# Optimization experiments

Measured on AMD Instinct MI355X. Metric: run time of the kernel, lower is better.

## Reference

```python
import jax, jax.numpy as jnp
import numpy as np
import math

D = 256; NH = 8; NG = 64; META = 6

def _linear(x, w, b):
    return x @ w.T + b

def setup_inputs():
    key = jax.random.key(0)
    ks = jax.random.split(key, 12)
    B, T, TG = 32, 4096, 1024
    def rn(k, shape, s=0.02):
        return jax.random.normal(k, shape, dtype=jnp.float32) * s
    q = jax.random.normal(ks[0], (1, NG, D), dtype=jnp.float32)
    q = q / jnp.clip(jnp.linalg.norm(q, axis=-1, keepdims=True), 1e-6)
    # fibonacci unit sphere anchor, scaled by 0.4
    idx = jnp.arange(NG, dtype=jnp.float32)
    golden = (1.0 + math.sqrt(5.0)) / 2.0
    theta = 2.0 * math.pi * idx / golden
    z = jnp.clip(1.0 - (2.0 * idx + 1.0) / NG, -1.0 + 1e-6, 1.0 - 1e-6)
    r = jnp.sqrt(jnp.clip(1.0 - z * z, 0.0))
    pts = jnp.stack([r * jnp.cos(theta), r * jnp.sin(theta), z], axis=-1)
    pts = pts / jnp.clip(jnp.linalg.norm(pts, axis=-1, keepdims=True), 1e-6)
    p0 = (pts * 0.4)[None]
    ph_b2 = jnp.array([0.0] * 6 + [-2.0] * 4, dtype=jnp.float32)
    return dict(
        local_feat=jax.random.normal(ks[1], (B, D, T), dtype=jnp.float32),
        global_feat=jax.random.normal(ks[2], (B, D, TG), dtype=jnp.float32),
        meta=jax.random.uniform(ks[3], (B, META), dtype=jnp.float32),
        queries=q, p0_anchor=p0,
        in_proj_w=rn(ks[4], (3 * D, D)), in_proj_b=jnp.zeros((3 * D,), jnp.float32),
        out_proj_w=rn(ks[5], (D, D)), out_proj_b=jnp.zeros((D,), jnp.float32),
        ln_g=jnp.ones((D,), jnp.float32), ln_b=jnp.zeros((D,), jnp.float32),
        meta_w=rn(ks[6], (D, META)), meta_b=jnp.zeros((D,), jnp.float32),
        temporal_w=rn(ks[7], (D, D)), temporal_b=jnp.zeros((D,), jnp.float32),
        shift_w=rn(ks[8], (3, D)), shift_b=jnp.zeros((3,), jnp.float32),
        ph_w1=rn(ks[9], (D // 2, D)), ph_b1=jnp.zeros((D // 2,), jnp.float32),
        ph_w2=rn(ks[10], (10, D // 2)), ph_b2=ph_b2,
        wave_delay_scale=jnp.float32(0.1),
        envelope_bias=jnp.float32(0.5),
    )

def reference(local_feat, global_feat, meta, queries, p0_anchor, in_proj_w, in_proj_b,
              out_proj_w, out_proj_b, ln_g, ln_b, meta_w, meta_b, temporal_w, temporal_b,
              shift_w, shift_b, ph_w1, ph_b1, ph_w2, ph_b2, wave_delay_scale, envelope_bias):
    B, _, T = local_feat.shape
    DH = D // NH
    kv = jnp.transpose(global_feat, (0, 2, 1))                        # [B,TG,D]
    q = jnp.broadcast_to(queries, (B, NG, D))
    wq, wk, wv = in_proj_w[:D], in_proj_w[D:2 * D], in_proj_w[2 * D:]
    bq, bk, bv = in_proj_b[:D], in_proj_b[D:2 * D], in_proj_b[2 * D:]
    qh = _linear(q, wq, bq).reshape(B, NG, NH, DH)
    kh = _linear(kv, wk, bk).reshape(B, -1, NH, DH)
    vh = _linear(kv, wv, bv).reshape(B, -1, NH, DH)
    attn = jax.nn.softmax(jnp.einsum('bqhd,bkhd->bhqk', qh, kh) / math.sqrt(DH), axis=-1)
    ctx = jnp.einsum('bhqk,bkhd->bqhd', attn, vh).reshape(B, NG, D)
    x = q + _linear(ctx, out_proj_w, out_proj_b)
    mu = x.mean(-1, keepdims=True)
    var = ((x - mu) ** 2).mean(-1, keepdims=True)
    q_static = (x - mu) / jnp.sqrt(var + 1e-5) * ln_g + ln_b
    q_static = q_static + jax.nn.gelu(_linear(meta, meta_w, meta_b), approximate=False)[:, None, :]
    params = _linear(jax.nn.gelu(_linear(q_static, ph_w1, ph_b1), approximate=False), ph_w2, ph_b2)
    p0_delta = jnp.tanh(params[..., 0:3]) * 0.2
    heart_shift = jnp.tanh(_linear(global_feat.mean(-1), shift_w, shift_b)) * 0.3
    p_pos = p0_anchor + p0_delta + heart_shift[:, None, :]            # [B,NG,3]
    dnorm = jnp.clip(jnp.linalg.norm(params[..., 3:6], axis=-1, keepdims=True), 1e-6)
    dipole_dir = params[..., 3:6] / dnorm
    volume_xyz = jax.nn.sigmoid(params[..., 6:9]) * 0.5 + 0.001
    amplitude = jax.nn.sigmoid(params[..., 9]) + 1e-4                 # [B,NG]
    tw = _linear(q_static, temporal_w, temporal_b)                    # [B,NG,D]
    temporal_logits = jnp.einsum('bnc,bct->bnt', tw, local_feat) / math.sqrt(D)
    idx_sa = jnp.argmax(amplitude, axis=1)                            # [B]
    p_sa = jnp.take_along_axis(p_pos, idx_sa[:, None, None], axis=1)  # [B,1,3]
    dist = jnp.linalg.norm(p_pos - p_sa, axis=-1)                     # [B,NG]
    delay = jnp.clip(jax.nn.softplus(wave_delay_scale) * dist, 0.0, 0.1)
    base_x = jnp.linspace(-1.0, 1.0, T)
    grid_x = base_x[None, None, :] - delay[..., None]                 # [B,NG,T]
    # grid_sample(bilinear, zeros, align_corners=True): grid_y hits rows exactly,
    # so it reduces to 1D linear interp along time with zero padding.
    x_pix = (grid_x + 1.0) * 0.5 * (T - 1)
    x0 = jnp.floor(x_pix).astype(jnp.int32)
    x1 = x0 + 1
    w1 = x_pix - x0.astype(x_pix.dtype)
    w0 = 1.0 - w1
    def samp(xi):
        g = jnp.take_along_axis(temporal_logits, jnp.clip(xi, 0, T - 1), axis=-1)
        return g * ((xi >= 0) & (xi <= T - 1)).astype(g.dtype)
    shifted = w0 * samp(x0) + w1 * samp(x1)
    envelope_t = jax.nn.sigmoid(shifted + envelope_bias)              # [B,NG,T]
    return amplitude, p_pos, dipole_dir, volume_xyz, envelope_t
```

## Files before the change

### kernel.cpp

```cpp
#include <hip/hip_runtime.h>
#include <hip/hip_bf16.h>
#include <math.h>

typedef __hip_bfloat16 bf16;
typedef short s16x8 __attribute__((ext_vector_type(8)));
typedef float f32x4 __attribute__((ext_vector_type(4)));

#define NDIM 256
#define NTG 1024
#define NT 4096

__device__ __forceinline__ float gelu_exact(float x) {
    return 0.5f * x * (1.0f + erff(x * 0.70710678118654752440f));
}
__device__ __forceinline__ float sigmoidf_(float x) {
    return 1.0f / (1.0f + __expf(-x));
}
__device__ __forceinline__ short f2bf_s(float x) {
    union { bf16 h; short s; } cv;
    cv.h = __float2bfloat16(x);
    return cv.s;
}
__device__ __forceinline__ float bf2f(short s) {
    union { bf16 h; short s; } cv;
    cv.s = s;
    return __bfloat162float(cv.h);
}

__global__ __launch_bounds__(256) void k_prep(
        const float* __restrict__ gf, const float* __restrict__ ipw,
        const float* __restrict__ opw, const float* __restrict__ twm,
        const float* __restrict__ pw1, const float* __restrict__ queries,
        const float* __restrict__ ipb,
        bf16* __restrict__ gfT, float* __restrict__ partial,
        float* __restrict__ opwT, float* __restrict__ twT, float* __restrict__ pw1T,
        bf16* __restrict__ wkvK, bf16* __restrict__ wkvV,
        float* __restrict__ qh) {
    __shared__ float smem[64 * 65 + 256];
    int blk = blockIdx.x, tid = threadIdx.x;
    if (blk < 2048) {
        float (*tile)[65] = (float(*)[65])smem;
        float* psum = smem + 64 * 65;
        int t0 = (blk & 15) * 64, c0 = ((blk >> 4) & 3) * 64, b = blk >> 6;
        int tt = tid & 63, ci = tid >> 6;
        #pragma unroll
        for (int r = 0; r < 16; ++r) {
            int cl = ci * 16 + r;
            tile[cl][tt] = gf[((size_t)(b * 256 + c0 + cl)) * NTG + t0 + tt];
        }
        __syncthreads();
        int cc = tid & 63, ti = tid >> 6;
        #pragma unroll
        for (int r = 0; r < 16; ++r) {
            int tl = ti * 16 + r;
            gfT[((size_t)(b * 1024 + t0 + tl)) * 256 + c0 + cc] =
                __float2bfloat16(tile[cc][tl]);
        }
        float ps = 0.f;
        #pragma unroll
        for (int r = 0; r < 16; ++r) ps += tile[cc][ti * 16 + r];
        psum[tid] = ps;
        __syncthreads();
        if (tid < 64) {
            float s = psum[tid] + psum[tid + 64] + psum[tid + 128] + psum[tid + 192];
            partial[(b * 256 + c0 + tid) * 16 + (blk & 15)] = s;
        }
    } else {
        int pblk = blk - 2048;
        if (pblk < 384) {
            int id = pblk * 256 + tid;
            if (id < 65536) {
                int k = id >> 8, c = id & 255;
                opwT[id] = opw[c * 256 + k];
                twT[id]  = twm[c * 256 + k];
            } else {
                int id2 = id - 65536;
                int k = id2 >> 7, m = id2 & 127;
                pw1T[id2] = pw1[m * 256 + k];
            }
        } else if (pblk < 640) {
            int id = (pblk - 384) * 256 + tid;
            wkvK[id] = __float2bfloat16(ipw[65536 + id]);
            wkvV[id] = __float2bfloat16(ipw[131072 + id]);
        } else {
            float* qrow = smem;
            int n = pblk - 640, c = tid;
            qrow[c] = queries[n * 256 + c];
            __syncthreads();
            float s = ipb[c];
            const float* wr = ipw + c * 256;
            for (int k = 0; k < 256; ++k) s += qrow[k] * wr[k];
            qh[n * 256 + c] = s;
        }
    }
}

__global__ __launch_bounds__(256) void k_kv(
        const short* __restrict__ gfT, const short* __restrict__ wkvK,
        const short* __restrict__ wkvV, const float* __restrict__ ipb,
        const float* __restrict__ meta, const float* __restrict__ mw,
        const float* __restrict__ mb, const float* __restrict__ partial,
        const float* __restrict__ sw, const float* __restrict__ sb,
        short* __restrict__ kvh, short* __restrict__ vTg,
        float* __restrict__ metag, float* __restrict__ hshift) {
    int blk = blockIdx.x;
    int tid = threadIdx.x;
    if (blk >= 512) {
        __shared__ float gm[256];
        int b = blk - 512, c = tid;
        float m = 0.f;
        const float* pp = partial + (b * 256 + c) * 16;
        #pragma unroll
        for (int tt = 0; tt < 16; ++tt) m += pp[tt];
        gm[c] = m * (1.0f / 1024.0f);
        float s = mb[c];
        #pragma unroll
        for (int j = 0; j < 6; ++j) s += meta[b * 6 + j] * mw[c * 6 + j];
        metag[b * 256 + c] = gelu_exact(s);
        __syncthreads();
        if (c < 3) {
            float t = sb[c];
            for (int k = 0; k < 256; ++k) t += gm[k] * sw[c * 256 + k];
            hshift[b * 4 + c] = tanhf(t) * 0.3f;
        }
        return;
    }
    int w = tid >> 6, lane = tid & 63, lm = lane & 15, quad = lane >> 4;
    int bx = blk & 7, sel = (blk >> 3) & 1, b = blk >> 4;
    int t0 = bx * 128 + w * 32;
    s16x8 g[8][2];
    #pragma unroll
    for (int ks = 0; ks < 8; ++ks) {
        int c = ks * 32 + quad * 8;
        #pragma unroll
        for (int mt = 0; mt < 2; ++mt)
            g[ks][mt] = *(const s16x8*)&gfT[((size_t)(b * 1024 + t0 + mt * 16 + lm)) * 256 + c];
    }
    if (sel == 0) {
        for (int n0i = 0; n0i < 4; ++n0i) {
            int n0 = n0i * 64;
            f32x4 acc[4][2];
            #pragma unroll
            for (int ni = 0; ni < 4; ++ni)
                #pragma unroll
                for (int mt = 0; mt < 2; ++mt) acc[ni][mt] = (f32x4)(0.0f);
            #pragma unroll
            for (int ks = 0; ks < 8; ++ks) {
                int c = ks * 32 + quad * 8;
                #pragma unroll
                for (int ni = 0; ni < 4; ++ni) {
                    s16x8 aw = *(const s16x8*)&wkvK[(n0 + ni * 16 + lm) * 256 + c];
                    #pragma unroll
                    for (int mt = 0; mt < 2; ++mt)
                        acc[ni][mt] = __builtin_amdgcn_mfma_f32_16x16x32_bf16(aw, g[ks][mt], acc[ni][mt], 0, 0, 0);
                }
            }
            #pragma unroll
            for (int ni = 0; ni < 4; ++ni) {
                int nb4 = n0 + ni * 16 + quad * 4;
                float4 bias = *(const float4*)&ipb[256 + nb4];
                #pragma unroll
                for (int mt = 0; mt < 2; ++mt) {
                    int t = t0 + mt * 16 + lm;
                    ushort4 o;
                    o.x = (unsigned short)f2bf_s(acc[ni][mt][0] + bias.x);
                    o.y = (unsigned short)f2bf_s(acc[ni][mt][1] + bias.y);
                    o.z = (unsigned short)f2bf_s(acc[ni][mt][2] + bias.z);
                    o.w = (unsigned short)f2bf_s(acc[ni][mt][3] + bias.w);
                    *(ushort4*)&kvh[((size_t)(b * 1024 + t)) * 256 + nb4] = o;
                }
            }
        }
    } else {
        for (int n0i = 0; n0i < 4; ++n0i) {
            int n0 = n0i * 64;
            f32x4 acc[2][4];
            #pragma unroll
            for (int mt = 0; mt < 2; ++mt)
                #pragma unroll
                for (int ni = 0; ni < 4; ++ni) acc[mt][ni] = (f32x4)(0.0f);
            #pragma unroll
            for (int ks = 0; ks < 8; ++ks) {
                int c = ks * 32 + quad * 8;
                #pragma unroll
                for (int ni = 0; ni < 4; ++ni) {
                    s16x8 bw = *(const s16x8*)&wkvV[(n0 + ni * 16 + lm) * 256 + c];
                    #pragma unroll
                    for (int mt = 0; mt < 2; ++mt)
                        acc[mt][ni] = __builtin_amdgcn_mfma_f32_16x16x32_bf16(g[ks][mt], bw, acc[mt][ni], 0, 0, 0);
                }
            }
            #pragma unroll
            for (int ni = 0; ni < 4; ++ni) {
                int nv = n0 + ni * 16 + lm;
                float bias = ipb[512 + nv];
                #pragma unroll
                for (int mt = 0; mt < 2; ++mt) {
                    int t4 = t0 + mt * 16 + quad * 4;
                    ushort4 o;
                    o.x = (unsigned short)f2bf_s(acc[mt][ni][0] + bias);
                    o.y = (unsigned short)f2bf_s(acc[mt][ni][1] + bias);
                    o.z = (unsigned short)f2bf_s(acc[mt][ni][2] + bias);
                    o.w = (unsigned short)f2bf_s(acc[mt][ni][3] + bias);
                    *(ushort4*)&vTg[((size_t)(b * 256 + nv)) * 1024 + t4] = o;
                }
            }
        }
    }
}

__global__ __launch_bounds__(256) void k_attn(
        const short* __restrict__ kvh, const short* __restrict__ vTg,
        const float* __restrict__ qh,
        float* __restrict__ o_half, float* __restrict__ l_half) {
    __shared__ short pT[4][64 * 40];
    __shared__ float obuf[4][64 * 36];
    __shared__ float lbuf[4 * 64];
    int tid = threadIdx.x;
    int w = tid >> 6, lane = tid & 63, lm = lane & 15, quad = lane >> 4;
    int half = blockIdx.x, h = blockIdx.y, b = blockIdx.z;
    s16x8 aq[4];
    #pragma unroll
    for (int mt = 0; mt < 4; ++mt) {
        const float4* qp = (const float4*)(qh + (mt * 16 + lm) * 256 + h * 32 + quad * 8);
        float4 qa = qp[0], qb = qp[1];
        aq[mt][0] = f2bf_s(qa.x); aq[mt][1] = f2bf_s(qa.y);
        aq[mt][2] = f2bf_s(qa.z); aq[mt][3] = f2bf_s(qa.w);
        aq[mt][4] = f2bf_s(qb.x); aq[mt][5] = f2bf_s(qb.y);
        aq[mt][6] = f2bf_s(qb.z); aq[mt][7] = f2bf_s(qb.w);
    }
    f32x4 acco[2][4];
    #pragma unroll
    for (int dt = 0; dt < 2; ++dt)
        #pragma unroll
        for (int qt = 0; qt < 4; ++qt) acco[dt][qt] = (f32x4)(0.0f);
    float lp[4][4];
    #pragma unroll
    for (int mt = 0; mt < 4; ++mt)
        #pragma unroll
        for (int r = 0; r < 4; ++r) lp[mt][r] = 0.f;
    const float scale = 0.17677669529663687f;
    int kb = half * 512 + w * 128;
    for (int ch = 0; ch < 4; ++ch) {
        int n0 = kb + ch * 32;
        #pragma unroll
        for (int nt = 0; nt < 2; ++nt) {
            int key = n0 + nt * 16 + lm;
            s16x8 bk = *(const s16x8*)&kvh[((size_t)(b * 1024 + key)) * 256 + h * 32 + quad * 8];
            f32x4 zero = {0.f, 0.f, 0.f, 0.f};
            #pragma unroll
            for (int mt = 0; mt < 4; ++mt) {
                f32x4 S = __builtin_amdgcn_mfma_f32_16x16x32_bf16(aq[mt], bk, zero, 0, 0, 0);
                #pragma unroll
                for (int r = 0; r < 4; ++r) {
                    float e = __expf(S[r] * scale);
                    lp[mt][r] += e;
                    pT[w][(mt * 16 + quad * 4 + r) * 40 + nt * 16 + lm] = f2bf_s(e);
                }
            }
        }
        s16x8 av[2], bp[4];
        #pragma unroll
        for (int dt = 0; dt < 2; ++dt)
            av[dt] = *(const s16x8*)&vTg[((size_t)(b * 256 + h * 32 + dt * 16 + lm)) * 1024 + n0 + quad * 8];
        #pragma unroll
        for (int qt = 0; qt < 4; ++qt)
            bp[qt] = *(const s16x8*)&pT[w][(qt * 16 + lm) * 40 + quad * 8];
        #pragma unroll
        for (int dt = 0; dt < 2; ++dt)
            #pragma unroll
            for (int qt = 0; qt < 4; ++qt)
                acco[dt][qt] = __builtin_amdgcn_mfma_f32_16x16x32_bf16(av[dt], bp[qt], acco[dt][qt], 0, 0, 0);
    }
    #pragma unroll
    for (int mt = 0; mt < 4; ++mt)
        #pragma unroll
        for (int r = 0; r < 4; ++r) {
            float v = lp[mt][r];
            v += __shfl_xor(v, 1); v += __shfl_xor(v, 2);
            v += __shfl_xor(v, 4); v += __shfl_xor(v, 8);
            lp[mt][r] = v;
        }
    #pragma unroll
    for (int dt = 0; dt < 2; ++dt)
        #pragma unroll
        for (int qt = 0; qt < 4; ++qt) {
            int q = qt * 16 + lm;
            float4 t;
            t.x = acco[dt][qt][0]; t.y = acco[dt][qt][1];
            t.z = acco[dt][qt][2]; t.w = acco[dt][qt][3];
            *(float4*)&obuf[w][q * 36 + dt * 16 + quad * 4] = t;
        }
    if (lm == 0) {
        #pragma unroll
        for (int mt = 0; mt < 4; ++mt)
            #pragma unroll
            for (int r = 0; r < 4; ++r)
                lbuf[w * 64 + mt * 16 + quad * 4 + r] = lp[mt][r];
    }
    __syncthreads();
    int q = tid & 63, dg = tid >> 6;
    int blk = (b * 8 + h) * 2 + half;
    float l = lbuf[q] + lbuf[64 + q] + lbuf[128 + q] + lbuf[192 + q];
    float o[8];
    #pragma unroll
    for (int j = 0; j < 8; ++j) o[j] = 0.f;
    #pragma unroll
    for (int w2 = 0; w2 < 4; ++w2) {
        const float* src = &obuf[w2][q * 36 + dg * 8];
        #pragma unroll
        for (int j = 0; j < 8; ++j) o[j] += src[j];
    }
    float* dst = &o_half[(((size_t)blk * 64) + q) * 32 + dg * 8];
    #pragma unroll
    for (int j = 0; j < 8; ++j) dst[j] = o[j];
    if (dg == 0) l_half[blk * 64 + q] = l;
}

__global__ __launch_bounds__(256) void k_post(
        const float* __restrict__ o_half, const float* __restrict__ l_half,
        const float* __restrict__ queries,
        const float* __restrict__ opwT, const float* __restrict__ opb,
        const float* __restrict__ lng, const float* __restrict__ lnb,
        const float* __restrict__ metag, const float* __restrict__ hshift,
        const float* __restrict__ twT, const float* __restrict__ tbv,
        const float* __restrict__ pw1T, const float* __restrict__ pb1,
        const float* __restrict__ pw2, const float* __restrict__ pb2,
        const float* __restrict__ p0a,
        bf16* __restrict__ twbf, float* __restrict__ out_amp,
        float* __restrict__ out_ppos, float* __restrict__ out_dip,
        float* __restrict__ out_vol) {
    __shared__ float cs[4][256];
    __shared__ float xs[4][256];
    __shared__ float qs[4][256];
    __shared__ float h1[4][128];
    __shared__ float ps[4][10];
    int tid = threadIdx.x;
    int n0 = blockIdx.x * 4, b = blockIdx.y;
    {
        int h = tid >> 5, d = tid & 31;
        int blk0 = (b * 8 + h) * 2;
        #pragma unroll
        for (int r = 0; r < 4; ++r) {
            int q = n0 + r;
            float l = l_half[blk0 * 64 + q] + l_half[(blk0 + 1) * 64 + q];
            float v0 = o_half[(((size_t)blk0 * 64) + q) * 32 + d];
            float v1 = o_half[(((size_t)(blk0 + 1) * 64) + q) * 32 + d];
            cs[r][tid] = (v0 + v1) / l;
        }
    }
    __syncthreads();
    {
        int c = tid;
        float a[4];
        #pragma unroll
        for (int nn = 0; nn < 4; ++nn) a[nn] = opb[c];
        for (int k = 0; k < 256; ++k) {
            float w = opwT[k * 256 + c];
            #pragma unroll
            for (int nn = 0; nn < 4; ++nn) a[nn] += cs[nn][k] * w;
        }
        #pragma unroll
        for (int nn = 0; nn < 4; ++nn)
            xs[nn][c] = queries[(n0 + nn) * 256 + c] + a[nn];
    }
    __syncthreads();
    {
        int w = tid >> 6, lane = tid & 63;
        int nr = w;
        float x0 = xs[nr][lane], x1 = xs[nr][lane + 64],
              x2 = xs[nr][lane + 128], x3 = xs[nr][lane + 192];
        float s = x0 + x1 + x2 + x3;
        #pragma unroll
        for (int off = 32; off >= 1; off >>= 1) s += __shfl_xor(s, off);
        float mu = s * (1.0f / 256.0f);
        float e0 = x0 - mu, e1 = x1 - mu, e2 = x2 - mu, e3 = x3 - mu;
        float v = e0*e0 + e1*e1 + e2*e2 + e3*e3;
        #pragma unroll
        for (int off = 32; off >= 1; off >>= 1) v += __shfl_xor(v, off);
        float rstd = 1.0f / sqrtf(v * (1.0f / 256.0f) + 1e-5f);
        #pragma unroll
        for (int j = 0; j < 4; ++j) {
            int c = lane + 64 * j;
            qs[nr][c] = (xs[nr][c] - mu) * rstd * lng[c] + lnb[c] + metag[b * 256 + c];
        }
    }
    __syncthreads();
    {
        int c = tid;
        float a[4];
        #pragma unroll
        for (int nn = 0; nn < 4; ++nn) a[nn] = tbv[c];
        for (int k = 0; k < 256; ++k) {
            float w = twT[k * 256 + c];
            #pragma unroll
            for (int nn = 0; nn < 4; ++nn) a[nn] += qs[nn][k] * w;
        }
        #pragma unroll
        for (int nn = 0; nn < 4; ++nn)
            twbf[(size_t)(b * 64 + n0 + nn) * 256 + c] = __float2bfloat16(a[nn]);
    }
    {
        int m = tid & 127, g = tid >> 7;
        float a[2];
        #pragma unroll
        for (int q2 = 0; q2 < 2; ++q2) a[q2] = pb1[m];
        for (int k = 0; k < 256; ++k) {
            float w = pw1T[k * 128 + m];
            #pragma unroll
            for (int q2 = 0; q2 < 2; ++q2) a[q2] += qs[g * 2 + q2][k] * w;
        }
        #pragma unroll
        for (int q2 = 0; q2 < 2; ++q2) h1[g * 2 + q2][m] = gelu_exact(a[q2]);
    }
    __syncthreads();
    if (tid < 40) {
        int nr = tid / 10, j = tid % 10;
        float s = pb2[j];
        for (int m = 0; m < 128; ++m) s += h1[nr][m] * pw2[j * 128 + m];
        ps[nr][j] = s;
    }
    __syncthreads();
    if (tid < 4) {
        int nr = tid;
        int gn = b * 64 + n0 + nr;
        #pragma unroll
        for (int j = 0; j < 3; ++j) {
            float delta = tanhf(ps[nr][j]) * 0.2f;
            out_ppos[gn * 3 + j] = p0a[(n0 + nr) * 3 + j] + delta + hshift[b * 4 + j];
        }
        float d0 = ps[nr][3], d1 = ps[nr][4], d2 = ps[nr][5];
        float dn = fmaxf(sqrtf(d0 * d0 + d1 * d1 + d2 * d2), 1e-6f);
        out_dip[gn * 3 + 0] = d0 / dn;
        out_dip[gn * 3 + 1] = d1 / dn;
        out_dip[gn * 3 + 2] = d2 / dn;
        #pragma unroll
        for (int j = 0; j < 3; ++j)
            out_vol[gn * 3 + j] = sigmoidf_(ps[nr][6 + j]) * 0.5f + 0.001f;
        out_amp[gn] = sigmoidf_(ps[nr][9]) + 0.0001f;
    }
}

__global__ __launch_bounds__(256) void k_temporal(
        const float* __restrict__ lf, const short* __restrict__ twbf,
        short* __restrict__ logits) {
    __shared__ __align__(16) short tws[64 * 264];
    __shared__ __align__(16) short lfs[2][32 * 132];
    int tid = threadIdx.x;
    int t0 = blockIdx.x * 128, b = blockIdx.y;
    int wave = tid >> 6, lane = tid & 63;
    int lm = lane & 15, quad = lane >> 4;

    #pragma unroll
    for (int i = 0; i < 8; ++i) {
        int id = i * 256 + tid;
        int n = id >> 5, c8 = id & 31;
        s16x8 v = *(const s16x8*)&twbf[(size_t)(b * 64 + n) * 256 + c8 * 8];
        *(s16x8*)&tws[n * 264 + c8 * 8] = v;
    }

    float4 fr[4];
    #pragma unroll
    for (int r = 0; r < 4; ++r) {
        int id = r * 256 + tid;
        int c = id >> 5, t4 = id & 31;
        fr[r] = *(const float4*)&lf[((size_t)(b * 256 + c)) * 4096 + t0 + t4 * 4];
    }
    #pragma unroll
    for (int r = 0; r < 4; ++r) {
        int id = r * 256 + tid;
        int c = id >> 5, t4 = id & 31;
        ushort4 o;
        o.x = (unsigned short)f2bf_s(fr[r].x);
        o.y = (unsigned short)f2bf_s(fr[r].y);
        o.z = (unsigned short)f2bf_s(fr[r].z);
        o.w = (unsigned short)f2bf_s(fr[r].w);
        *(ushort4*)&lfs[0][c * 132 + t4 * 4] = o;
    }

    f32x4 acc[2][4];
    #pragma unroll
    for (int mi = 0; mi < 2; ++mi)
        #pragma unroll
        for (int ni = 0; ni < 4; ++ni) acc[mi][ni] = (f32x4)(0.0f);

    __syncthreads();

    for (int ksi = 0; ksi < 8; ++ksi) {
        int cur = ksi & 1;
        if (ksi < 7) {
            int c0n = (ksi + 1) * 32;
            #pragma unroll
            for (int r = 0; r < 4; ++r) {
                int id = r * 256 + tid;
                int c = id >> 5, t4 = id & 31;
                fr[r] = *(const float4*)&lf[((size_t)(b * 256 + c0n + c)) * 4096 + t0 + t4 * 4];
            }
        }
        int c0 = ksi * 32;
        #pragma unroll
        for (int mi = 0; mi < 2; ++mi) {
            int tl = wave * 32 + mi * 16 + lm;
            s16x8 af;
            #pragma unroll
            for (int j = 0; j < 8; ++j)
                af[j] = lfs[cur][(quad * 8 + j) * 132 + tl];
            #pragma unroll
            for (int ni = 0; ni < 4; ++ni) {
                s16x8 bfr = *(const s16x8*)&tws[(ni * 16 + lm) * 264 + c0 + quad * 8];
                acc[mi][ni] = __builtin_amdgcn_mfma_f32_16x16x32_bf16(af, bfr, acc[mi][ni], 0, 0, 0);
            }
        }
        if (ksi < 7) {
            #pragma unroll
            for (int r = 0; r < 4; ++r) {
                int id = r * 256 + tid;
                int c = id >> 5, t4 = id & 31;
                ushort4 o;
                o.x = (unsigned short)f2bf_s(fr[r].x);
                o.y = (unsigned short)f2bf_s(fr[r].y);
                o.z = (unsigned short)f2bf_s(fr[r].z);
                o.w = (unsigned short)f2bf_s(fr[r].w);
                *(ushort4*)&lfs[cur ^ 1][c * 132 + t4 * 4] = o;
            }
        }
        __syncthreads();
    }
    #pragma unroll
    for (int mi = 0; mi < 2; ++mi) {
        #pragma unroll
        for (int ni = 0; ni < 4; ++ni) {
            int n = ni * 16 + lm;
            int t = t0 + wave * 32 + mi * 16 + quad * 4;
            ushort4 o;
            o.x = (unsigned short)f2bf_s(acc[mi][ni][0] * 0.0625f);
            o.y = (unsigned short)f2bf_s(acc[mi][ni][1] * 0.0625f);
            o.z = (unsigned short)f2bf_s(acc[mi][ni][2] * 0.0625f);
            o.w = (unsigned short)f2bf_s(acc[mi][ni][3] * 0.0625f);
            *(ushort4*)&logits[(size_t)(b * 64 + n) * 4096 + t] = o;
        }
    }
}

__global__ __launch_bounds__(256) void k_envelope(
        const short* __restrict__ logits,
        const float* __restrict__ out_amp,
        const float* __restrict__ out_ppos,
        const float* __restrict__ wds,
        const float* __restrict__ ebp,
        float* __restrict__ env) {
    __shared__ __align__(16) short ls[208 + 4096 + 16];
    int bn = blockIdx.x;
    int b = bn >> 6, n = bn & 63;
    int tid = threadIdx.x;
    int lane = tid & 63;
    if (tid < 208) ls[tid] = 0;
    if (tid < 16) ls[208 + 4096 + tid] = 0;
    const short* gl = logits + (size_t)bn * 4096;
    {
        s16x8 v0 = *(const s16x8*)&gl[tid * 16];
        s16x8 v1 = *(const s16x8*)&gl[tid * 16 + 8];
        *(s16x8*)&ls[208 + tid * 16] = v0;
        *(s16x8*)&ls[208 + tid * 16 + 8] = v1;
    }
    float v = out_amp[b * 64 + lane];
    int idx = lane;
    #pragma unroll
    for (int off = 1; off < 64; off <<= 1) {
        float ov = __shfl_xor(v, off);
        int oi = __shfl_xor(idx, off);
        if (ov > v || (ov == v && oi < idx)) { v = ov; idx = oi; }
    }
    float dx = out_ppos[(b * 64 + n) * 3 + 0] - out_ppos[(b * 64 + idx) * 3 + 0];
    float dy = out_ppos[(b * 64 + n) * 3 + 1] - out_ppos[(b * 64 + idx) * 3 + 1];
    float dz = out_ppos[(b * 64 + n) * 3 + 2] - out_ppos[(b * 64 + idx) * 3 + 2];
    float dist = sqrtf(dx * dx + dy * dy + dz * dz);
    float sp = log1pf(expf(wds[0]));
    float dl = fminf(fmaxf(sp * dist, 0.f), 0.1f);
    float eb = ebp[0];
    __syncthreads();
    #pragma unroll
    for (int g = 0; g < 4; ++g) {
        int t_base = g * 1024 + tid * 4;
        float ov4[4];
        #pragma unroll
        for (int u = 0; u < 4; ++u) {
            int t = t_base + u;
            float xb = fmaf((float)t, 2.0f / 4095.0f, -1.0f);
            float xp = (xb - dl + 1.0f) * 2047.5f;
            float x0f = floorf(xp);
            int x0 = (int)x0f;
            float w1 = xp - x0f, w0 = 1.0f - w1;
            float g0 = bf2f(ls[208 + x0]);
            float g1 = bf2f(ls[208 + x0 + 1]);
            float sh = w0 * g0 + w1 * g1;
            ov4[u] = 1.0f / (1.0f + __expf(-(sh + eb)));
        }
        float4 o; o.x = ov4[0]; o.y = ov4[1]; o.z = ov4[2]; o.w = ov4[3];
        *reinterpret_cast<float4*>(&env[(size_t)bn * 4096 + t_base]) = o;
    }
}

extern "C" void kernel_launch(void* const* d_in, const int* in_sizes, int n_in,
                              void* d_out, int out_size, void* d_ws, size_t ws_size,
                              hipStream_t stream) {
    const float* lf   = (const float*)d_in[0];
    const float* gf   = (const float*)d_in[1];
    const float* meta = (const float*)d_in[2];
    const float* qrs  = (const float*)d_in[3];
    const float* p0a  = (const float*)d_in[4];
    const float* ipw  = (const float*)d_in[5];
    const float* ipb  = (const float*)d_in[6];
    const float* opw  = (const float*)d_in[7];
    const float* opb  = (const float*)d_in[8];
    const float* lng  = (const float*)d_in[9];
    const float* lnb  = (const float*)d_in[10];
    const float* mw   = (const float*)d_in[11];
    const float* mb   = (const float*)d_in[12];
    const float* twm  = (const float*)d_in[13];
    const float* tbv  = (const float*)d_in[14];
    const float* sw   = (const float*)d_in[15];
    const float* sb   = (const float*)d_in[16];
    const float* pw1  = (const float*)d_in[17];
    const float* pb1  = (const float*)d_in[18];
    const float* pw2  = (const float*)d_in[19];
    const float* pb2  = (const float*)d_in[20];
    const float* wds  = (const float*)d_in[21];
    const float* ebp  = (const float*)d_in[22];

    char* ws = (char*)d_ws;
    short* kvh    = (short*)(ws);
    short* vTg    = (short*)(ws + 16777216);
    short* gfT    = (short*)(ws + 33554432);
    short* logits = (short*)(ws + 50331648);
    float* o_half = (float*)(ws + 67108864);
    float* l_half = (float*)(ws + 71303168);
    short* twbf   = (short*)(ws + 71434240);
    float* qh     = (float*)(ws + 72482816);
    float* metag  = (float*)(ws + 72581120);
    float* hshift = (float*)(ws + 72613888);
    float* opwT   = (float*)(ws + 72614400);
    float* twT    = (float*)(ws + 72876544);
    float* pw1T   = (float*)(ws + 73138688);
    short* wkvK   = (short*)(ws + 73269760);
    short* wkvV   = (short*)(ws + 73400832);
    float* partial= (float*)(ws + 73531904);

    float* out_amp  = (float*)d_out;
    float* out_ppos = out_amp + 2048;
    float* out_dip  = out_amp + 8192;
    float* out_vol  = out_amp + 14336;
    float* env      = out_amp + 20480;

    k_prep<<<2752, 256, 0, stream>>>(gf, ipw, opw, twm, pw1, qrs, ipb,
                                     (bf16*)gfT, partial, opwT, twT, pw1T,
                                     (bf16*)wkvK, (bf16*)wkvV, qh);
    k_kv<<<544, 256, 0, stream>>>(gfT, wkvK, wkvV, ipb, meta, mw, mb, partial,
                                  sw, sb, kvh, vTg, metag, hshift);
    k_attn<<<dim3(2, 8, 32), 256, 0, stream>>>(kvh, vTg, qh, o_half, l_half);
    k_post<<<dim3(16, 32), 256, 0, stream>>>(o_half, l_half, qrs, opwT, opb, lng, lnb,
                                             metag, hshift, twT, tbv, pw1T, pb1, pw2, pb2,
                                             p0a, (bf16*)twbf, out_amp, out_ppos,
                                             out_dip, out_vol);
    k_temporal<<<dim3(32, 32), 256, 0, stream>>>(lf, twbf, logits);
    k_envelope<<<2048, 256, 0, stream>>>(logits, out_amp, out_ppos, wds, ebp, env);
}
```

Before: 389.0 us.

## Fuse global-feature transpose and bf16 convert into KV projection kernel

Removes the separate transpose pass that wrote a bf16 transposed copy of global_feat to workspace. The KV projection kernel now loads fp32 global_feat directly, converts and transposes it into shared memory, computes the per-channel partial sums with wave shuffles, and then computes both K and V projections from the same shared tile. The meta/shift side computation moves from the KV kernel into extra blocks of the attention kernel. This saves a full write and read of the transposed intermediate and one grid's worth of work, at the cost of heavier per-block shared-memory staging and strided LDS stores.

```diff
diff --git a/kernel.cpp b/kernel.cpp
--- a/kernel.cpp
+++ b/kernel.cpp
@@ -28,91 +28,156 @@
 }
 
 __global__ __launch_bounds__(256) void k_prep(
-        const float* __restrict__ gf, const float* __restrict__ ipw,
-        const float* __restrict__ opw, const float* __restrict__ twm,
-        const float* __restrict__ pw1, const float* __restrict__ queries,
-        const float* __restrict__ ipb,
-        bf16* __restrict__ gfT, float* __restrict__ partial,
+        const float* __restrict__ ipw, const float* __restrict__ opw,
+        const float* __restrict__ twm, const float* __restrict__ pw1,
+        const float* __restrict__ queries, const float* __restrict__ ipb,
         float* __restrict__ opwT, float* __restrict__ twT, float* __restrict__ pw1T,
         bf16* __restrict__ wkvK, bf16* __restrict__ wkvV,
         float* __restrict__ qh) {
-    __shared__ float smem[64 * 65 + 256];
+    __shared__ float qrow[256];
     int blk = blockIdx.x, tid = threadIdx.x;
-    if (blk < 2048) {
-        float (*tile)[65] = (float(*)[65])smem;
-        float* psum = smem + 64 * 65;
-        int t0 = (blk & 15) * 64, c0 = ((blk >> 4) & 3) * 64, b = blk >> 6;
-        int tt = tid & 63, ci = tid >> 6;
-        #pragma unroll
-        for (int r = 0; r < 16; ++r) {
-            int cl = ci * 16 + r;
-            tile[cl][tt] = gf[((size_t)(b * 256 + c0 + cl)) * NTG + t0 + tt];
-        }
+    if (blk < 384) {
+        int id = blk * 256 + tid;
+        if (id < 65536) {
+            int k = id >> 8, c = id & 255;
+            opwT[id] = opw[c * 256 + k];
+            twT[id]  = twm[c * 256 + k];
+        } else {
+            int id2 = id - 65536;
+            int k = id2 >> 7, m = id2 & 127;
+            pw1T[id2] = pw1[m * 256 + k];
+        }
+    } else if (blk < 640) {
+        int id = (blk - 384) * 256 + tid;
+        wkvK[id] = __float2bfloat16(ipw[65536 + id]);
+        wkvV[id] = __float2bfloat16(ipw[131072 + id]);
+    } else {
+        int n = blk - 640, c = tid;
+        qrow[c] = queries[n * 256 + c];
         __syncthreads();
-        int cc = tid & 63, ti = tid >> 6;
-        #pragma unroll
-        for (int r = 0; r < 16; ++r) {
-            int tl = ti * 16 + r;
-            gfT[((size_t)(b * 1024 + t0 + tl)) * 256 + c0 + cc] =
-                __float2bfloat16(tile[cc][tl]);
-        }
-        float ps = 0.f;
-        #pragma unroll
-        for (int r = 0; r < 16; ++r) ps += tile[cc][ti * 16 + r];
-        psum[tid] = ps;
-        __syncthreads();
-        if (tid < 64) {
-            float s = psum[tid] + psum[tid + 64] + psum[tid + 128] + psum[tid + 192];
-            partial[(b * 256 + c0 + tid) * 16 + (blk & 15)] = s;
-        }
-    } else {
-        int pblk = blk - 2048;
-        if (pblk < 384) {
-            int id = pblk * 256 + tid;
-            if (id < 65536) {
-                int k = id >> 8, c = id & 255;
-                opwT[id] = opw[c * 256 + k];
-                twT[id]  = twm[c * 256 + k];
-            } else {
-                int id2 = id - 65536;
-                int k = id2 >> 7, m = id2 & 127;
-                pw1T[id2] = pw1[m * 256 + k];
-            }
-        } else if (pblk < 640) {
-            int id = (pblk - 384) * 256 + tid;
-            wkvK[id] = __float2bfloat16(ipw[65536 + id]);
-            wkvV[id] = __float2bfloat16(ipw[131072 + id]);
-        } else {
-            float* qrow = smem;
-            int n = pblk - 640, c = tid;
-            qrow[c] = queries[n * 256 + c];
-            __syncthreads();
-            float s = ipb[c];
-            const float* wr = ipw + c * 256;
-            for (int k = 0; k < 256; ++k) s += qrow[k] * wr[k];
-            qh[n * 256 + c] = s;
-        }
+        float s = ipb[c];
+        const float* wr = ipw + c * 256;
+        for (int k = 0; k < 256; ++k) s += qrow[k] * wr[k];
+        qh[n * 256 + c] = s;
     }
 }
 
 __global__ __launch_bounds__(256) void k_kv(
-        const short* __restrict__ gfT, const short* __restrict__ wkvK,
+        const float* __restrict__ gf, const short* __restrict__ wkvK,
         const short* __restrict__ wkvV, const float* __restrict__ ipb,
+        short* __restrict__ kvh, short* __restrict__ vTg,
+        float* __restrict__ partial) {
+    __shared__ __align__(16) short gfs[64 * 264];
+    int blk = blockIdx.x, tid = threadIdx.x;
+    int b = blk >> 4, tt = blk & 15;
+    int t0 = tt * 64;
+    int f4 = tid & 15, grp = tid >> 4;
+    #pragma unroll 4
+    for (int p = 0; p < 16; ++p) {
+        int row = p * 16 + grp;
+        float4 v = *(const float4*)&gf[((size_t)(b * 256 + row)) * 1024 + t0 + f4 * 4];
+        gfs[(f4 * 4 + 0) * 264 + row] = f2bf_s(v.x);
+        gfs[(f4 * 4 + 1) * 264 + row] = f2bf_s(v.y);
+        gfs[(f4 * 4 + 2) * 264 + row] = f2bf_s(v.z);
+        gfs[(f4 * 4 + 3) * 264 + row] = f2bf_s(v.w);
+        float ps = v.x + v.y + v.z + v.w;
+        ps += __shfl_xor(ps, 1); ps += __shfl_xor(ps, 2);
+        ps += __shfl_xor(ps, 4); ps += __shfl_xor(ps, 8);
+        if (f4 == 0) partial[(b * 256 + row) * 16 + tt] = ps;
+    }
+    __syncthreads();
+    int w = tid >> 6, lane = tid & 63, lm = lane & 15, quad = lane >> 4;
+    int n0 = w * 64;
+    f32x4 acc[4][4];
+    #pragma unroll
+    for (int ni = 0; ni < 4; ++ni)
+        #pragma unroll
+        for (int mt = 0; mt < 4; ++mt) acc[ni][mt] = (f32x4)(0.0f);
+    #pragma unroll
+    for (int ks = 0; ks < 8; ++ks) {
+        int c = ks * 32 + quad * 8;
+        s16x8 gm[4];
+        #pragma unroll
+        for (int mt = 0; mt < 4; ++mt)
+            gm[mt] = *(const s16x8*)&gfs[(mt * 16 + lm) * 264 + c];
+        #pragma unroll
+        for (int ni = 0; ni < 4; ++ni) {
+            s16x8 aw = *(const s16x8*)&wkvK[(n0 + ni * 16 + lm) * 256 + c];
+            #pragma unroll
+            for (int mt = 0; mt < 4; ++mt)
+                acc[ni][mt] = __builtin_amdgcn_mfma_f32_16x16x32_bf16(aw, gm[mt], acc[ni][mt], 0, 0, 0);
+        }
+    }
+    #pragma unroll
+    for (int ni = 0; ni < 4; ++ni) {
+        int nb4 = n0 + ni * 16 + quad * 4;
+        float4 bias = *(const float4*)&ipb[256 + nb4];
+        #pragma unroll
+        for (int mt = 0; mt < 4; ++mt) {
+            int t = t0 + mt * 16 + lm;
+            ushort4 o;
+            o.x = (unsigned short)f2bf_s(acc[ni][mt][0] + bias.x);
+            o.y = (unsigned short)f2bf_s(acc[ni][mt][1] + bias.y);
+            o.z = (unsigned short)f2bf_s(acc[ni][mt][2] + bias.z);
+            o.w = (unsigned short)f2bf_s(acc[ni][mt][3] + bias.w);
+            *(ushort4*)&kvh[((size_t)(b * 1024 + t)) * 256 + nb4] = o;
+        }
+    }
+    #pragma unroll
+    for (int mt = 0; mt < 4; ++mt)
+        #pragma unroll
+        for (int ni = 0; ni < 4; ++ni) acc[mt][ni] = (f32x4)(0.0f);
+    #pragma unroll
+    for (int ks = 0; ks < 8; ++ks) {
+        int c = ks * 32 + quad * 8;
+        s16x8 gm[4];
+        #pragma unroll
+        for (int mt = 0; mt < 4; ++mt)
+            gm[mt] = *(const s16x8*)&gfs[(mt * 16 + lm) * 264 + c];
+        #pragma unroll
+        for (int ni = 0; ni < 4; ++ni) {
+            s16x8 bw = *(const s16x8*)&wkvV[(n0 + ni * 16 + lm) * 256 + c];
+            #pragma unroll
+            for (int mt = 0; mt < 4; ++mt)
+                acc[mt][ni] = __builtin_amdgcn_mfma_f32_16x16x32_bf16(gm[mt], bw, acc[mt][ni], 0, 0, 0);
+        }
+    }
+    #pragma unroll
+    for (int ni = 0; ni < 4; ++ni) {
+        int nv = n0 + ni * 16 + lm;
+        float bias = ipb[512 + nv];
+        #pragma unroll
+        for (int mt = 0; mt < 4; ++mt) {
+            int t4 = t0 + mt * 16 + quad * 4;
+            ushort4 o;
+            o.x = (unsigned short)f2bf_s(acc[mt][ni][0] + bias);
+            o.y = (unsigned short)f2bf_s(acc[mt][ni][1] + bias);
+            o.z = (unsigned short)f2bf_s(acc[mt][ni][2] + bias);
+            o.w = (unsigned short)f2bf_s(acc[mt][ni][3] + bias);
+            *(ushort4*)&vTg[((size_t)(b * 256 + nv)) * 1024 + t4] = o;
+        }
+    }
+}
+
+__global__ __launch_bounds__(256) void k_attn(
+        const short* __restrict__ kvh, const short* __restrict__ vTg,
+        const float* __restrict__ qh,
         const float* __restrict__ meta, const float* __restrict__ mw,
         const float* __restrict__ mb, const float* __restrict__ partial,
         const float* __restrict__ sw, const float* __restrict__ sb,
-        short* __restrict__ kvh, short* __restrict__ vTg,
+        float* __restrict__ o_half, float* __restrict__ l_half,
         float* __restrict__ metag, float* __restrict__ hshift) {
-    int blk = blockIdx.x;
-    int tid = threadIdx.x;
-    if (blk >= 512) {
-        __shared__ float gm[256];
-        int b = blk - 512, c = tid;
+    __shared__ short pT[4][64 * 40];
+    __shared__ float obuf[4][64 * 36];
+    __shared__ float lbuf[4 * 64];
+    if (blockIdx.z >= 32) {
+        int b = (blockIdx.z - 32) * 16 + blockIdx.y * 2 + blockIdx.x;
+        int c = threadIdx.x;
         float m = 0.f;
         const float* pp = partial + (b * 256 + c) * 16;
         #pragma unroll
-        for (int tt = 0; tt < 16; ++tt) m += pp[tt];
-        gm[c] = m * (1.0f / 1024.0f);
+        for (int t = 0; t < 16; ++t) m += pp[t];
+        lbuf[c] = m * (1.0f / 1024.0f);
         float s = mb[c];
         #pragma unroll
         for (int j = 0; j < 6; ++j) s += meta[b * 6 + j] * mw[c * 6 + j];
@@ -120,102 +185,11 @@
         __syncthreads();
         if (c < 3) {
             float t = sb[c];
-            for (int k = 0; k < 256; ++k) t += gm[k] * sw[c * 256 + k];
+            for (int k = 0; k < 256; ++k) t += lbuf[k] * sw[c * 256 + k];
             hshift[b * 4 + c] = tanhf(t) * 0.3f;
         }
         return;
     }
-    int w = tid >> 6, lane = tid & 63, lm = lane & 15, quad = lane >> 4;
-    int bx = blk & 7, sel = (blk >> 3) & 1, b = blk >> 4;
-    int t0 = bx * 128 + w * 32;
-    s16x8 g[8][2];
-    #pragma unroll
-    for (int ks = 0; ks < 8; ++ks) {
-        int c = ks * 32 + quad * 8;
-        #pragma unroll
-        for (int mt = 0; mt < 2; ++mt)
-            g[ks][mt] = *(const s16x8*)&gfT[((size_t)(b * 1024 + t0 + mt * 16 + lm)) * 256 + c];
-    }
-    if (sel == 0) {
-        for (int n0i = 0; n0i < 4; ++n0i) {
-            int n0 = n0i * 64;
-            f32x4 acc[4][2];
-            #pragma unroll
-            for (int ni = 0; ni < 4; ++ni)
-                #pragma unroll
-                for (int mt = 0; mt < 2; ++mt) acc[ni][mt] = (f32x4)(0.0f);
-            #pragma unroll
-            for (int ks = 0; ks < 8; ++ks) {
-                int c = ks * 32 + quad * 8;
-                #pragma unroll
-                for (int ni = 0; ni < 4; ++ni) {
-                    s16x8 aw = *(const s16x8*)&wkvK[(n0 + ni * 16 + lm) * 256 + c];
-                    #pragma unroll
-                    for (int mt = 0; mt < 2; ++mt)
-                        acc[ni][mt] = __builtin_amdgcn_mfma_f32_16x16x32_bf16(aw, g[ks][mt], acc[ni][mt], 0, 0, 0);
-                }
-            }
-            #pragma unroll
-            for (int ni = 0; ni < 4; ++ni) {
-                int nb4 = n0 + ni * 16 + quad * 4;
-                float4 bias = *(const float4*)&ipb[256 + nb4];
-                #pragma unroll
-                for (int mt = 0; mt < 2; ++mt) {
-                    int t = t0 + mt * 16 + lm;
-                    ushort4 o;
-                    o.x = (unsigned short)f2bf_s(acc[ni][mt][0] + bias.x);
-                    o.y = (unsigned short)f2bf_s(acc[ni][mt][1] + bias.y);
-                    o.z = (unsigned short)f2bf_s(acc[ni][mt][2] + bias.z);
-                    o.w = (unsigned short)f2bf_s(acc[ni][mt][3] + bias.w);
-                    *(ushort4*)&kvh[((size_t)(b * 1024 + t)) * 256 + nb4] = o;
-                }
-            }
-        }
-    } else {
-        for (int n0i = 0; n0i < 4; ++n0i) {
-            int n0 = n0i * 64;
-            f32x4 acc[2][4];
-            #pragma unroll
-            for (int mt = 0; mt < 2; ++mt)
-                #pragma unroll
-                for (int ni = 0; ni < 4; ++ni) acc[mt][ni] = (f32x4)(0.0f);
-            #pragma unroll
-            for (int ks = 0; ks < 8; ++ks) {
-                int c = ks * 32 + quad * 8;
-                #pragma unroll
-                for (int ni = 0; ni < 4; ++ni) {
-                    s16x8 bw = *(const s16x8*)&wkvV[(n0 + ni * 16 + lm) * 256 + c];
-                    #pragma unroll
-                    for (int mt = 0; mt < 2; ++mt)
-                        acc[mt][ni] = __builtin_amdgcn_mfma_f32_16x16x32_bf16(g[ks][mt], bw, acc[mt][ni], 0, 0, 0);
-                }
-            }
-            #pragma unroll
-            for (int ni = 0; ni < 4; ++ni) {
-                int nv = n0 + ni * 16 + lm;
-                float bias = ipb[512 + nv];
-                #pragma unroll
-                for (int mt = 0; mt < 2; ++mt) {
-                    int t4 = t0 + mt * 16 + quad * 4;
-                    ushort4 o;
-                    o.x = (unsigned short)f2bf_s(acc[mt][ni][0] + bias);
-                    o.y = (unsigned short)f2bf_s(acc[mt][ni][1] + bias);
-                    o.z = (unsigned short)f2bf_s(acc[mt][ni][2] + bias);
-                    o.w = (unsigned short)f2bf_s(acc[mt][ni][3] + bias);
-                    *(ushort4*)&vTg[((size_t)(b * 256 + nv)) * 1024 + t4] = o;
-                }
-            }
-        }
-    }
-}
-
-__global__ __launch_bounds__(256) void k_attn(
-        const short* __restrict__ kvh, const short* __restrict__ vTg,
-        const float* __restrict__ qh,
-        float* __restrict__ o_half, float* __restrict__ l_half) {
-    __shared__ short pT[4][64 * 40];
-    __shared__ float obuf[4][64 * 36];
-    __shared__ float lbuf[4 * 64];
     int tid = threadIdx.x;
     int w = tid >> 6, lane = tid & 63, lm = lane & 15, quad = lane >> 4;
     int half = blockIdx.x, h = blockIdx.y, b = blockIdx.z;
@@ -631,7 +605,6 @@
     char* ws = (char*)d_ws;
     short* kvh    = (short*)(ws);
     short* vTg    = (short*)(ws + 16777216);
-    short* gfT    = (short*)(ws + 33554432);
     short* logits = (short*)(ws + 50331648);
     float* o_half = (float*)(ws + 67108864);
     float* l_half = (float*)(ws + 71303168);
@@ -652,12 +625,11 @@
     float* out_vol  = out_amp + 14336;
     float* env      = out_amp + 20480;
 
-    k_prep<<<2752, 256, 0, stream>>>(gf, ipw, opw, twm, pw1, qrs, ipb,
-                                     (bf16*)gfT, partial, opwT, twT, pw1T,
-                                     (bf16*)wkvK, (bf16*)wkvV, qh);
-    k_kv<<<544, 256, 0, stream>>>(gfT, wkvK, wkvV, ipb, meta, mw, mb, partial,
-                                  sw, sb, kvh, vTg, metag, hshift);
-    k_attn<<<dim3(2, 8, 32), 256, 0, stream>>>(kvh, vTg, qh, o_half, l_half);
+    k_prep<<<704, 256, 0, stream>>>(ipw, opw, twm, pw1, qrs, ipb,
+                                    opwT, twT, pw1T, (bf16*)wkvK, (bf16*)wkvV, qh);
+    k_kv<<<512, 256, 0, stream>>>(gf, wkvK, wkvV, ipb, kvh, vTg, partial);
+    k_attn<<<dim3(2, 8, 34), 256, 0, stream>>>(kvh, vTg, qh, meta, mw, mb, partial,
+                                               sw, sb, o_half, l_half, metag, hshift);
     k_post<<<dim3(16, 32), 256, 0, stream>>>(o_half, l_half, qrs, opwT, opb, lng, lnb,
                                              metag, hshift, twT, tbv, pw1T, pb1, pw2, pb2,
                                              p0a, (bf16*)twbf, out_amp, out_ppos,
```

Measured after the change: 371.6 us. 4.5% less time.
